# Optimization experiments

Hardware: AMD Instinct MI355X
Metric: run time of the kernel (lower is better)

The kernel has to match this reference:

```python
import jax, jax.numpy as jnp
import numpy as np

N_NODES = 50000
N_EDGES = 800000
HID = 128
LAYERS = 3


def setup_inputs() -> dict:
    key = jax.random.key(0)
    k1, k2, k3, k4 = jax.random.split(key, 4)
    x = jax.random.normal(k1, (N_NODES, HID), dtype=jnp.float32)
    edge_index = jax.random.randint(k2, (2, N_EDGES), 0, N_NODES, dtype=jnp.int64)
    # Glorot-ish scale so 3 stacked layers stay numerically tame
    Ws = jax.random.normal(k3, (LAYERS, HID, HID), dtype=jnp.float32) * (1.0 / np.sqrt(HID))
    bs = jax.random.normal(k4, (LAYERS, HID), dtype=jnp.float32) * 0.01
    return {"x": x, "edge_index": edge_index, "Ws": Ws, "bs": bs}


def reference(x, edge_index, Ws, bs):
    """Stacked GCNConv (add_self_loops=False): out = D^-1/2 A D^-1/2 (x W) + b.
    Returns (final_x, embeddings_list) like the torch module."""
    N = x.shape[0]
    src = edge_index[0]  # message sources (x_j)
    dst = edge_index[1]  # aggregation targets
    # gcn_norm with unit edge weights, no self loops: in-degree on targets
    deg = jax.ops.segment_sum(jnp.ones(src.shape[0], dtype=x.dtype), dst, num_segments=N)
    dinv = jnp.where(deg > 0, jax.lax.rsqrt(jnp.maximum(deg, 1.0)), 0.0).astype(x.dtype)
    norm = dinv[src] * dinv[dst]  # [E]

    embeddings = [x]
    for l in range(Ws.shape[0]):
        h = x @ Ws[l]                               # [N, D] dense transform
        msg = h[src] * norm[:, None]                # [E, D] gather + normalize
        x = jax.ops.segment_sum(msg, dst, num_segments=N) + bs[l]  # scatter-add
        embeddings.append(x)
    return (x, embeddings)
```

## Files before the change

kernel.cpp:

```cpp
#include <hip/hip_runtime.h>

#define N_NODES 50000
#define N_EDGES 800000
#define HID 128
#define SLOT (N_NODES * HID)
#define W_STRIDE (HID * HID)

#define OFF_CNT    0ul
#define OFF_DINV   200192ul
#define OFF_RPTR   400384ul
#define OFF_RFILL  600576ul
#define OFF_BSUM   800768ul
#define OFF_BOFS   801792ul
#define OFF_SRCS   802816ul
#define OFF_H_WS   4002816ul


__global__ void k_count(const int* __restrict__ ei, int* __restrict__ cnt,
                        const float* __restrict__ x, float* __restrict__ slot1) {
    int g = blockIdx.x * blockDim.x + threadIdx.x;
    if (g < N_EDGES) atomicAdd(&cnt[ei[N_EDGES + g]], 1);
    const float4* x4  = (const float4*)x;
    float4*       s14 = (float4*)slot1;
    int gs = gridDim.x * blockDim.x;
    for (int i = g; i < SLOT / 4; i += gs) s14[i] = x4[i];
}

__global__ void k_scan_block(const int* __restrict__ cnt, int* __restrict__ rptr,
                             int* __restrict__ bsum) {
    __shared__ int s[512];
    int tid = threadIdx.x;
    int gid = blockIdx.x * 512 + tid;
    int v = (gid < N_NODES) ? cnt[gid] : 0;
    s[tid] = v;
    __syncthreads();
    for (int off = 1; off < 512; off <<= 1) {
        int t = (tid >= off) ? s[tid - off] : 0;
        __syncthreads();
        s[tid] += t;
        __syncthreads();
    }
    if (gid < N_NODES) rptr[gid] = s[tid] - v;
    if (tid == 511) bsum[blockIdx.x] = s[511];
}

__global__ void k_scan_sums(const int* __restrict__ bsum, int* __restrict__ bofs, int nb) {
    __shared__ int s[128];
    int tid = threadIdx.x;
    int v = (tid < nb) ? bsum[tid] : 0;
    s[tid] = v;
    __syncthreads();
    for (int off = 1; off < 128; off <<= 1) {
        int t = (tid >= off) ? s[tid - off] : 0;
        __syncthreads();
        s[tid] += t;
        __syncthreads();
    }
    if (tid < nb) bofs[tid] = s[tid] - v;
}

__global__ void k_scan_add(int* __restrict__ rptr, int* __restrict__ rfill,
                           const int* __restrict__ bofs, const int* __restrict__ cnt,
                           float* __restrict__ dinv) {
    int gid = blockIdx.x * blockDim.x + threadIdx.x;
    if (gid < N_NODES) {
        int r = rptr[gid] + bofs[gid >> 9];
        rptr[gid] = r;
        rfill[gid] = r;
        int c = cnt[gid];
        dinv[gid] = (c > 0) ? rsqrtf((float)c) : 0.0f;
    }
    if (gid == 0) rptr[N_NODES] = N_EDGES;
}

__global__ void k_scatter(const int* __restrict__ ei, int* __restrict__ rfill,
                          int* __restrict__ srcs) {
    int e = blockIdx.x * blockDim.x + threadIdx.x;
    if (e < N_EDGES) {
        int sv = ei[e];
        int d  = ei[N_EDGES + e];
        int pos = atomicAdd(&rfill[d], 1);
        srcs[pos] = sv;
    }
}

__global__ void k_copy(const float* __restrict__ src, float* __restrict__ dst, int n4) {
    int i = blockIdx.x * blockDim.x + threadIdx.x;
    if (i < n4) ((float4*)dst)[i] = ((const float4*)src)[i];
}

__launch_bounds__(256, 2)
__global__ void k_gemm_scale(const float* __restrict__ X, const float* __restrict__ W,
                             const float* __restrict__ dinv, float* __restrict__ H) {
    __shared__ float sW[HID * 64];
    __shared__ float sX[64 * HID];
    int tid   = threadIdx.x;
    int chalf = blockIdx.x & 1;
    int row0  = (blockIdx.x >> 1) * 64;

    const float4* W4  = (const float4*)W;
    float4*       sW4 = (float4*)sW;
    for (int j = tid; j < 2048; j += 256) {
        int k  = j >> 4;
        int c4 = j & 15;
        sW4[j] = W4[k * 32 + chalf * 16 + c4];
    }

    const float4* X4  = (const float4*)X;
    float4*       sX4 = (float4*)sX;
    for (int j = tid; j < 2048; j += 256) {
        int r   = j >> 5;
        int c4  = j & 31;
        int row = row0 + r;
        float4 v = {0.f, 0.f, 0.f, 0.f};
        if (row < N_NODES) v = X4[row * 32 + c4];
        sX4[r * 32 + (c4 ^ ((r >> 3) & 7))] = v;
    }
    __syncthreads();

    int ty  = tid >> 4;
    int tx  = tid & 15;
    int swz = (ty >> 1) & 7;

    float4 acc[4];
    #pragma unroll
    for (int r = 0; r < 4; ++r) acc[r] = {0.f, 0.f, 0.f, 0.f};

    #pragma unroll 4
    for (int k0 = 0; k0 < HID; k0 += 4) {
        int k4 = k0 >> 2;
        float4 wv[4];
        #pragma unroll
        for (int kk = 0; kk < 4; ++kk)
            wv[kk] = sW4[(k0 + kk) * 16 + tx];
        float4 xv[4];
        #pragma unroll
        for (int r = 0; r < 4; ++r)
            xv[r] = sX4[(ty * 4 + r) * 32 + (k4 ^ swz)];
        #pragma unroll
        for (int r = 0; r < 4; ++r) {
            float xk0 = xv[r].x, xk1 = xv[r].y, xk2 = xv[r].z, xk3 = xv[r].w;
            acc[r].x += xk0 * wv[0].x + xk1 * wv[1].x + xk2 * wv[2].x + xk3 * wv[3].x;
            acc[r].y += xk0 * wv[0].y + xk1 * wv[1].y + xk2 * wv[2].y + xk3 * wv[3].y;
            acc[r].z += xk0 * wv[0].z + xk1 * wv[1].z + xk2 * wv[2].z + xk3 * wv[3].z;
            acc[r].w += xk0 * wv[0].w + xk1 * wv[1].w + xk2 * wv[2].w + xk3 * wv[3].w;
        }
    }

    float4* H4 = (float4*)H;
    #pragma unroll
    for (int r = 0; r < 4; ++r) {
        int row = row0 + ty * 4 + r;
        if (row < N_NODES) {
            float dv = dinv[row];
            float4 o = acc[r];
            o.x *= dv; o.y *= dv; o.z *= dv; o.w *= dv;
            H4[row * 32 + chalf * 16 + tx] = o;
        }
    }
}

__global__ void k_agg(const float* __restrict__ H, const int* __restrict__ rptr,
                      const int* __restrict__ srcs, const float* __restrict__ dinv,
                      const float* __restrict__ bias, float* __restrict__ out0,
                      float* __restrict__ out1) {
    int pair = (blockIdx.x * blockDim.x + threadIdx.x) >> 6;
    int lane = threadIdx.x & 63;
    int wid  = pair * 2 + (lane >> 5);
    int l32  = lane & 31;
    if (wid >= N_NODES) return;

    int beg = rptr[wid];
    int end = rptr[wid + 1];

    const float4* H4 = (const float4*)H;

    float4 a0 = {0.f,0.f,0.f,0.f}, a1 = {0.f,0.f,0.f,0.f};
    float4 a2 = {0.f,0.f,0.f,0.f}, a3 = {0.f,0.f,0.f,0.f};

    int p  = beg;
    int n4 = beg + ((end - beg) & ~3);
    for (; p < n4; p += 4) {
        int s0 = srcs[p + 0];
        int s1 = srcs[p + 1];
        int s2 = srcs[p + 2];
        int s3 = srcs[p + 3];
        float4 h0 = H4[s0 * 32 + l32];
        float4 h1 = H4[s1 * 32 + l32];
        float4 h2 = H4[s2 * 32 + l32];
        float4 h3 = H4[s3 * 32 + l32];
        a0.x += h0.x; a0.y += h0.y; a0.z += h0.z; a0.w += h0.w;
        a1.x += h1.x; a1.y += h1.y; a1.z += h1.z; a1.w += h1.w;
        a2.x += h2.x; a2.y += h2.y; a2.z += h2.z; a2.w += h2.w;
        a3.x += h3.x; a3.y += h3.y; a3.z += h3.z; a3.w += h3.w;
    }
    for (; p < end; ++p) {
        float4 hv = H4[srcs[p] * 32 + l32];
        a0.x += hv.x; a0.y += hv.y; a0.z += hv.z; a0.w += hv.w;
    }

    float dv  = dinv[wid];
    float4 bb = ((const float4*)bias)[l32];
    float4 res;
    res.x = (a0.x + a1.x + a2.x + a3.x) * dv + bb.x;
    res.y = (a0.y + a1.y + a2.y + a3.y) * dv + bb.y;
    res.z = (a0.z + a1.z + a2.z + a3.z) * dv + bb.z;
    res.w = (a0.w + a1.w + a2.w + a3.w) * dv + bb.w;
    ((float4*)out0)[wid * 32 + l32] = res;
    if (out1) ((float4*)out1)[wid * 32 + l32] = res;
}


extern "C" void kernel_launch(void* const* d_in, const int* in_sizes, int n_in,
                              void* d_out, int out_size, void* d_ws, size_t ws_size,
                              hipStream_t stream) {
    const float* x  = (const float*)d_in[0];
    const int*   ei = (const int*)d_in[1];
    const float* Ws = (const float*)d_in[2];
    const float* bs = (const float*)d_in[3];
    float* out = (float*)d_out;
    char*  ws  = (char*)d_ws;

    int*   cnt   = (int*)  (ws + OFF_CNT);
    float* dinv  = (float*)(ws + OFF_DINV);
    int*   rptr  = (int*)  (ws + OFF_RPTR);
    int*   rfill = (int*)  (ws + OFF_RFILL);
    int*   bsum  = (int*)  (ws + OFF_BSUM);
    int*   bofs  = (int*)  (ws + OFF_BOFS);
    int*   srcs  = (int*)  (ws + OFF_SRCS);

    float* slot0 = out;
    float* slot1 = out + 1l * SLOT;
    float* slot2 = out + 2l * SLOT;
    float* slot3 = out + 3l * SLOT;
    float* slot4 = out + 4l * SLOT;

    bool   h_in_ws = ws_size >= (size_t)(OFF_H_WS + (size_t)SLOT * 4);
    float* h = h_in_ws ? (float*)(ws + OFF_H_WS) : slot0;

    const int NB_NODE = (N_NODES + 255) / 256;
    const int NB_EDGE = (N_EDGES + 255) / 256;
    const int NB_SCAN = (N_NODES + 511) / 512;

    hipMemsetAsync(cnt, 0, N_NODES * sizeof(int), stream);
    k_count     <<<NB_EDGE, 256, 0, stream>>>(ei, cnt, x, slot1);
    k_scan_block<<<NB_SCAN, 512, 0, stream>>>(cnt, rptr, bsum);
    k_scan_sums <<<1, 128, 0, stream>>>(bsum, bofs, NB_SCAN);
    k_scan_add  <<<NB_NODE, 256, 0, stream>>>(rptr, rfill, bofs, cnt, dinv);
    k_scatter   <<<NB_EDGE, 256, 0, stream>>>(ei, rfill, srcs);

    const int NB_GEMM = 2 * ((N_NODES + 63) / 64);
    const int NB_AGG  = (N_NODES / 2 + 3) / 4;

    k_gemm_scale<<<NB_GEMM, 256, 0, stream>>>(x, Ws + 0 * W_STRIDE, dinv, h);
    k_agg       <<<NB_AGG, 256, 0, stream>>>(h, rptr, srcs, dinv, bs + 0 * HID, slot2, nullptr);

    k_gemm_scale<<<NB_GEMM, 256, 0, stream>>>(slot2, Ws + 1 * W_STRIDE, dinv, h);
    k_agg       <<<NB_AGG, 256, 0, stream>>>(h, rptr, srcs, dinv, bs + 1 * HID, slot3, nullptr);

    k_gemm_scale<<<NB_GEMM, 256, 0, stream>>>(slot3, Ws + 2 * W_STRIDE, dinv, h);
    if (h_in_ws) {
        k_agg<<<NB_AGG, 256, 0, stream>>>(h, rptr, srcs, dinv, bs + 2 * HID, slot4, slot0);
    } else {
        k_agg<<<NB_AGG, 256, 0, stream>>>(h, rptr, srcs, dinv, bs + 2 * HID, slot4, nullptr);
        k_copy<<<SLOT / 4 / 256, 256, 0, stream>>>(slot4, slot0, SLOT / 4);
    }
}
```

Before: 396.7 us.

## Fuse input copy into first GEMM, merge scan kernels, use nontemporal stores

```diff
diff --git a/kernel.cpp b/kernel.cpp
--- a/kernel.cpp
+++ b/kernel.cpp
@@ -5,25 +5,22 @@
 #define HID 128
 #define SLOT (N_NODES * HID)
 #define W_STRIDE (HID * HID)
+#define NCHUNK 98
+
+typedef float f32x4 __attribute__((ext_vector_type(4)));
 
 #define OFF_CNT    0ul
 #define OFF_DINV   200192ul
 #define OFF_RPTR   400384ul
 #define OFF_RFILL  600576ul
 #define OFF_BSUM   800768ul
-#define OFF_BOFS   801792ul
 #define OFF_SRCS   802816ul
 #define OFF_H_WS   4002816ul
 
 
-__global__ void k_count(const int* __restrict__ ei, int* __restrict__ cnt,
-                        const float* __restrict__ x, float* __restrict__ slot1) {
-    int g = blockIdx.x * blockDim.x + threadIdx.x;
-    if (g < N_EDGES) atomicAdd(&cnt[ei[N_EDGES + g]], 1);
-    const float4* x4  = (const float4*)x;
-    float4*       s14 = (float4*)slot1;
-    int gs = gridDim.x * blockDim.x;
-    for (int i = g; i < SLOT / 4; i += gs) s14[i] = x4[i];
+__global__ void k_count(const int* __restrict__ ei, int* __restrict__ cnt) {
+    int e = blockIdx.x * blockDim.x + threadIdx.x;
+    if (e < N_EDGES) atomicAdd(&cnt[ei[N_EDGES + e]], 1);
 }
 
 __global__ void k_scan_block(const int* __restrict__ cnt, int* __restrict__ rptr,
@@ -44,28 +41,25 @@
     if (tid == 511) bsum[blockIdx.x] = s[511];
 }
 
-__global__ void k_scan_sums(const int* __restrict__ bsum, int* __restrict__ bofs, int nb) {
-    __shared__ int s[128];
+__global__ void k_scan_add(int* __restrict__ rptr, int* __restrict__ rfill,
+                           const int* __restrict__ bsum, const int* __restrict__ cnt,
+                           float* __restrict__ dinv) {
+    __shared__ int sb[128];
     int tid = threadIdx.x;
-    int v = (tid < nb) ? bsum[tid] : 0;
-    s[tid] = v;
+    if (tid < 128) sb[tid] = (tid < NCHUNK) ? bsum[tid] : 0;
     __syncthreads();
     for (int off = 1; off < 128; off <<= 1) {
-        int t = (tid >= off) ? s[tid - off] : 0;
-        __syncthreads();
-        s[tid] += t;
-        __syncthreads();
-    }
-    if (tid < nb) bofs[tid] = s[tid] - v;
-}
-
-__global__ void k_scan_add(int* __restrict__ rptr, int* __restrict__ rfill,
-                           const int* __restrict__ bofs, const int* __restrict__ cnt,
-                           float* __restrict__ dinv) {
-    int gid = blockIdx.x * blockDim.x + threadIdx.x;
+        int t = (tid < 128 && tid >= off) ? sb[tid - off] : 0;
+        __syncthreads();
+        if (tid < 128) sb[tid] += t;
+        __syncthreads();
+    }
+    int gid = blockIdx.x * blockDim.x + tid;
     if (gid < N_NODES) {
-        int r = rptr[gid] + bofs[gid >> 9];
-        rptr[gid] = r;
+        int chunk = gid >> 9;
+        int base  = (chunk == 0) ? 0 : sb[chunk - 1];
+        int r = rptr[gid] + base;
+        rptr[gid]  = r;
         rfill[gid] = r;
         int c = cnt[gid];
         dinv[gid] = (c > 0) ? rsqrtf((float)c) : 0.0f;
@@ -91,7 +85,8 @@
 
 __launch_bounds__(256, 2)
 __global__ void k_gemm_scale(const float* __restrict__ X, const float* __restrict__ W,
-                             const float* __restrict__ dinv, float* __restrict__ H) {
+                             const float* __restrict__ dinv, float* __restrict__ H,
+                             float* __restrict__ copy_out) {
     __shared__ float sW[HID * 64];
     __shared__ float sX[64 * HID];
     int tid   = threadIdx.x;
@@ -108,12 +103,18 @@
 
     const float4* X4  = (const float4*)X;
     float4*       sX4 = (float4*)sX;
+    bool do_copy = (copy_out != nullptr) && (chalf == 0);
     for (int j = tid; j < 2048; j += 256) {
         int r   = j >> 5;
         int c4  = j & 31;
         int row = row0 + r;
         float4 v = {0.f, 0.f, 0.f, 0.f};
-        if (row < N_NODES) v = X4[row * 32 + c4];
+        if (row < N_NODES) {
+            v = X4[row * 32 + c4];
+            if (do_copy)
+                __builtin_nontemporal_store(*(const f32x4*)&v,
+                                            (f32x4*)&((float4*)copy_out)[row * 32 + c4]);
+        }
         sX4[r * 32 + (c4 ^ ((r >> 3) & 7))] = v;
     }
     __syncthreads();
@@ -206,8 +207,10 @@
     res.y = (a0.y + a1.y + a2.y + a3.y) * dv + bb.y;
     res.z = (a0.z + a1.z + a2.z + a3.z) * dv + bb.z;
     res.w = (a0.w + a1.w + a2.w + a3.w) * dv + bb.w;
-    ((float4*)out0)[wid * 32 + l32] = res;
-    if (out1) ((float4*)out1)[wid * 32 + l32] = res;
+
+    __builtin_nontemporal_store(*(const f32x4*)&res, (f32x4*)&((float4*)out0)[wid * 32 + l32]);
+    if (out1)
+        __builtin_nontemporal_store(*(const f32x4*)&res, (f32x4*)&((float4*)out1)[wid * 32 + l32]);
 }
 
 
@@ -226,7 +229,6 @@
     int*   rptr  = (int*)  (ws + OFF_RPTR);
     int*   rfill = (int*)  (ws + OFF_RFILL);
     int*   bsum  = (int*)  (ws + OFF_BSUM);
-    int*   bofs  = (int*)  (ws + OFF_BOFS);
     int*   srcs  = (int*)  (ws + OFF_SRCS);
 
     float* slot0 = out;
@@ -243,22 +245,21 @@
     const int NB_SCAN = (N_NODES + 511) / 512;
 
     hipMemsetAsync(cnt, 0, N_NODES * sizeof(int), stream);
-    k_count     <<<NB_EDGE, 256, 0, stream>>>(ei, cnt, x, slot1);
+    k_count     <<<NB_EDGE, 256, 0, stream>>>(ei, cnt);
     k_scan_block<<<NB_SCAN, 512, 0, stream>>>(cnt, rptr, bsum);
-    k_scan_sums <<<1, 128, 0, stream>>>(bsum, bofs, NB_SCAN);
-    k_scan_add  <<<NB_NODE, 256, 0, stream>>>(rptr, rfill, bofs, cnt, dinv);
+    k_scan_add  <<<NB_NODE, 256, 0, stream>>>(rptr, rfill, bsum, cnt, dinv);
     k_scatter   <<<NB_EDGE, 256, 0, stream>>>(ei, rfill, srcs);
 
     const int NB_GEMM = 2 * ((N_NODES + 63) / 64);
     const int NB_AGG  = (N_NODES / 2 + 3) / 4;
 
-    k_gemm_scale<<<NB_GEMM, 256, 0, stream>>>(x, Ws + 0 * W_STRIDE, dinv, h);
+    k_gemm_scale<<<NB_GEMM, 256, 0, stream>>>(x, Ws + 0 * W_STRIDE, dinv, h, slot1);
     k_agg       <<<NB_AGG, 256, 0, stream>>>(h, rptr, srcs, dinv, bs + 0 * HID, slot2, nullptr);
 
-    k_gemm_scale<<<NB_GEMM, 256, 0, stream>>>(slot2, Ws + 1 * W_STRIDE, dinv, h);
+    k_gemm_scale<<<NB_GEMM, 256, 0, stream>>>(slot2, Ws + 1 * W_STRIDE, dinv, h, nullptr);
     k_agg       <<<NB_AGG, 256, 0, stream>>>(h, rptr, srcs, dinv, bs + 1 * HID, slot3, nullptr);
 
-    k_gemm_scale<<<NB_GEMM, 256, 0, stream>>>(slot3, Ws + 2 * W_STRIDE, dinv, h);
+    k_gemm_scale<<<NB_GEMM, 256, 0, stream>>>(slot3, Ws + 2 * W_STRIDE, dinv, h, nullptr);
     if (h_in_ws) {
         k_agg<<<NB_AGG, 256, 0, stream>>>(h, rptr, srcs, dinv, bs + 2 * HID, slot4, slot0);
     } else {
```

Result: slower. 405.6 us (+2.3%).
